# Kernel tuning notes

Measured on AMD Instinct MI355X. Metric: run time of the kernel, lower is better.

## Reference

```python
import jax, jax.numpy as jnp
import numpy as np

I, H, P, B = 1024, 2048, 512, 8192


def setup_inputs() -> dict:
    key = jax.random.key(0)
    ks = jax.random.split(key, 8)
    return {
        "input": jax.random.normal(ks[0], (B, I), dtype=jnp.float32),
        "hx": jax.random.normal(ks[1], (B, P), dtype=jnp.float32),
        "cx": jax.random.normal(ks[2], (B, H), dtype=jnp.float32),
        # gate params stacked in (i, f, c, o) order -> [4H, ...]
        "w_x": jax.random.normal(ks[3], (4 * H, I), dtype=jnp.float32),
        "b_x": jax.random.normal(ks[4], (4 * H,), dtype=jnp.float32),
        "w_h": jax.random.normal(ks[5], (4 * H, P), dtype=jnp.float32),
        "b_h": jax.random.normal(ks[6], (4 * H,), dtype=jnp.float32),
        "w_proj": jax.random.normal(ks[7], (P, H), dtype=jnp.float32),
    }


def reference(input, hx, cx, w_x, b_x, w_h, b_h, w_proj):
    # One fused GEMM per operand instead of 8 small ones; same math.
    # gates: [B, 4H]
    gates = input @ w_x.T + b_x + hx @ w_h.T + b_h
    i_g, f_g, c_g, o_g = jnp.split(gates, 4, axis=-1)  # each [B, H]
    # NOTE: original module applies NO sigmoid/tanh to the gates (faithful).
    ct = f_g * cx + i_g * c_g                 # [B, H]
    ht = (o_g * jnp.tanh(ct)) @ w_proj.T       # [B, P]
    return (ht, ct)
```

## Files before the change

kernel.cpp:

```cpp
#include <hip/hip_runtime.h>
#include <math.h>
#include <stdint.h>

#define DI static __device__ __forceinline__

typedef __bf16 bf16x8 __attribute__((ext_vector_type(8)));
typedef float f32x4 __attribute__((ext_vector_type(4)));
typedef float float4v __attribute__((ext_vector_type(4)));
typedef unsigned short u16;
typedef unsigned short u16x4 __attribute__((ext_vector_type(4)));

DI float b2f(u16 s) {
    unsigned u = ((unsigned)s) << 16;
    float f;
    __builtin_memcpy(&f, &u, 4);
    return f;
}
DI u16 f2b(float f) {
    unsigned x;
    __builtin_memcpy(&x, &f, 4);
    unsigned r = x + 0x7FFFu + ((x >> 16) & 1u);
    return (u16)(r >> 16);
}

DI void gl_lds(const u16* g, u16* l) {
    __builtin_amdgcn_global_load_lds(
        (__attribute__((address_space(1))) void*)g,
        (__attribute__((address_space(3))) void*)l,
        16, 0, 0);
}

DI float fast_tanh(float x) {
    float xc = fminf(fmaxf(x, -15.f), 15.f);
    float e = __expf(2.0f * xc);
    return (e - 1.f) / (e + 1.f);
}

__global__ void pack_A(const float* __restrict__ inp, const float* __restrict__ hx,
                       u16* __restrict__ Ahi, u16* __restrict__ Alo) {
    const int r = blockIdx.x;
    const int k = threadIdx.x * 4;
    float4v v = (k < 1024) ? *(const float4v*)(inp + (size_t)r * 1024 + k)
                           : *(const float4v*)(hx + (size_t)r * 512 + (k - 1024));
    u16x4 h, l;
#pragma unroll
    for (int e = 0; e < 4; ++e) {
        h[e] = f2b(v[e]);
        l[e] = f2b(v[e] - b2f(h[e]));
    }
    *(u16x4*)(Ahi + (size_t)r * 1536 + k) = h;
    *(u16x4*)(Alo + (size_t)r * 1536 + k) = l;
}

__global__ void pack_W(const float* __restrict__ wx, const float* __restrict__ wh,
                       u16* __restrict__ Whi, u16* __restrict__ Wlo) {
    const int g = blockIdx.x;
    const int k = threadIdx.x * 4;
    float4v v = (k < 1024) ? *(const float4v*)(wx + (size_t)g * 1024 + k)
                           : *(const float4v*)(wh + (size_t)g * 512 + (k - 1024));
    u16x4 h, l;
#pragma unroll
    for (int e = 0; e < 4; ++e) {
        h[e] = f2b(v[e]);
        l[e] = f2b(v[e] - b2f(h[e]));
    }
    *(u16x4*)(Whi + (size_t)g * 1536 + k) = h;
    int lr = -1;
    if (g < 2048) lr = g;
    else if (g >= 4096 && g < 6144) lr = g - 2048;
    if (lr >= 0) *(u16x4*)(Wlo + (size_t)lr * 1536 + k) = l;
}

__global__ void pack_flat_bf16(const float* __restrict__ src, u16* __restrict__ dst) {
    const size_t t = ((size_t)blockIdx.x * blockDim.x + threadIdx.x) * 4;
    float4v v = *(const float4v*)(src + t);
    u16x4 o;
#pragma unroll
    for (int e = 0; e < 4; ++e) o[e] = f2b(v[e]);
    *(u16x4*)(dst + t) = o;
}

DI void swizzle2048(int id, int& bx, int& by) {
    const int xcd = id & 7;
    const int j = id >> 3;
    bx = xcd * 4 + (j & 3);
    by = j >> 2;
}

__global__ __launch_bounds__(256, 2) void gemm_fo(const u16* __restrict__ A,
                                                  const u16* __restrict__ W,
                                                  const float* __restrict__ bxv,
                                                  const float* __restrict__ bhv,
                                                  u16* __restrict__ out) {
    constexpr int K = 1536, BK = 32;
    constexpr int AB = 128 * BK;
    __shared__ u16 As[2 * AB];
    __shared__ u16 Ws[2 * AB];

    const int tid = threadIdx.x, wave = tid >> 6, lane = tid & 63;
    int bxi, byi;
    swizzle2048(blockIdx.x, bxi, byi);
    const size_t tileM = (size_t)byi * 128;
    const size_t wrow0 = (bxi < 16) ? (2048 + (size_t)bxi * 128)
                                    : (6144 + (size_t)(bxi - 16) * 128);
    const size_t ncol0 = (size_t)bxi * 128;
    const int waveM = (wave >> 1) * 64;
    const int waveN = (wave & 1) * 64;

    const int srow = lane >> 2, scol = (lane & 3) * 8;
    const u16* Ag = A + (tileM + (size_t)(wave * 16 + srow)) * K + scol;
    const u16* Wg = W + (wrow0 + (size_t)(wave * 16 + srow)) * K + scol;
    const int lA0 = (wave * 16) * BK;
    const int lA1 = (wave * 16 + 64) * BK;

    f32x4 acc[4][4] = {};
    const int arow = waveM + (lane & 15);
    const int wrow = waveN + (lane & 15);
    const int kq = (lane >> 4) * 8;

#define STAGE_FO(b, k0)                              \
    do {                                             \
        gl_lds(Ag + (k0), &As[(b)*AB + lA0]);        \
        gl_lds(Ag + (size_t)64 * K + (k0), &As[(b)*AB + lA1]); \
        gl_lds(Wg + (k0), &Ws[(b)*AB + lA0]);        \
        gl_lds(Wg + (size_t)64 * K + (k0), &Ws[(b)*AB + lA1]); \
    } while (0)

#define COMPUTE_FO(b)                                                          \
    do {                                                                       \
        bf16x8 af[4], wf[4];                                                   \
        _Pragma("unroll") for (int i = 0; i < 4; ++i)                          \
            af[i] = *(const bf16x8*)&As[(b)*AB + (arow + i * 16) * BK + kq];   \
        _Pragma("unroll") for (int j = 0; j < 4; ++j)                          \
            wf[j] = *(const bf16x8*)&Ws[(b)*AB + (wrow + j * 16) * BK + kq];   \
        _Pragma("unroll") for (int i = 0; i < 4; ++i)                          \
            _Pragma("unroll") for (int j = 0; j < 4; ++j)                      \
                acc[i][j] = __builtin_amdgcn_mfma_f32_16x16x32_bf16(           \
                    af[i], wf[j], acc[i][j], 0, 0, 0);                         \
    } while (0)

    STAGE_FO(0, 0);
    __syncthreads();
    for (int k0 = 0; k0 < K; k0 += 2 * BK) {
        STAGE_FO(1, k0 + BK);
        COMPUTE_FO(0);
        __syncthreads();
        if (k0 + 2 * BK < K) STAGE_FO(0, k0 + 2 * BK);
        COMPUTE_FO(1);
        __syncthreads();
    }
#undef STAGE_FO
#undef COMPUTE_FO

    const int rq = (lane >> 4) * 4;
#pragma unroll
    for (int i = 0; i < 4; ++i) {
        const size_t rbase = tileM + waveM + i * 16 + rq;
#pragma unroll
        for (int j = 0; j < 4; ++j) {
            const int nl = waveN + (lane & 15) + j * 16;
            const float bias = bxv[wrow0 + nl] + bhv[wrow0 + nl];
#pragma unroll
            for (int v = 0; v < 4; ++v)
                out[(rbase + v) * 4096 + ncol0 + nl] = f2b(acc[i][j][v] + bias);
        }
    }
}

__global__ __launch_bounds__(256, 2) void gemm_ic_cell(
    const u16* __restrict__ Ahi, const u16* __restrict__ Alo,
    const u16* __restrict__ Whi, const u16* __restrict__ Wlo,
    const float* __restrict__ bxv, const float* __restrict__ bhv,
    const u16* __restrict__ Gfo, const float* __restrict__ cx,
    float* __restrict__ ct, u16* __restrict__ U) {
    constexpr int K = 1536, BK = 32;
    constexpr int AB = 128 * BK;
    constexpr int WB = 64 * BK;
    __shared__ u16 sAh[2 * AB], sAl[2 * AB];
    __shared__ u16 sWih[2 * WB], sWil[2 * WB], sWch[2 * WB], sWcl[2 * WB];

    const int tid = threadIdx.x, wave = tid >> 6, lane = tid & 63;
    int bxi, byi;
    swizzle2048(blockIdx.x, bxi, byi);
    const size_t tileM = (size_t)byi * 128;
    const size_t h0 = (size_t)bxi * 64;
    const int waveM = (wave >> 1) * 64;
    const int waveH = (wave & 1) * 32;

    const int srow = lane >> 2, scol = (lane & 3) * 8;
    const size_t wr = (size_t)(wave * 16 + srow);
    const u16* gAh = Ahi + (tileM + wr) * K + scol;
    const u16* gAl = Alo + (tileM + wr) * K + scol;
    const u16* gWih = Whi + (h0 + wr) * K + scol;
    const u16* gWch = Whi + (4096 + h0 + wr) * K + scol;
    const u16* gWil = Wlo + (h0 + wr) * K + scol;
    const u16* gWcl = Wlo + (2048 + h0 + wr) * K + scol;
    const int lA0 = (wave * 16) * BK;
    const int lA1 = (wave * 16 + 64) * BK;
    const int lW0 = (wave * 16) * BK;

    f32x4 ai[4][2] = {}, ac[4][2] = {};
    const int arow = waveM + (lane & 15);
    const int wrow = waveH + (lane & 15);
    const int kq = (lane >> 4) * 8;

#define STAGE_IC(b, k0)                                          \
    do {                                                         \
        gl_lds(gAh + (k0), &sAh[(b)*AB + lA0]);                  \
        gl_lds(gAh + (size_t)64 * K + (k0), &sAh[(b)*AB + lA1]); \
        gl_lds(gAl + (k0), &sAl[(b)*AB + lA0]);                  \
        gl_lds(gAl + (size_t)64 * K + (k0), &sAl[(b)*AB + lA1]); \
        gl_lds(gWih + (k0), &sWih[(b)*WB + lW0]);                \
        gl_lds(gWil + (k0), &sWil[(b)*WB + lW0]);                \
        gl_lds(gWch + (k0), &sWch[(b)*WB + lW0]);                \
        gl_lds(gWcl + (k0), &sWcl[(b)*WB + lW0]);                \
    } while (0)

#define COMPUTE_IC(b)                                                            \
    do {                                                                         \
        bf16x8 ah[4], al[4], wih[2], wil[2], wch[2], wcl[2];                     \
        _Pragma("unroll") for (int i = 0; i < 4; ++i) {                          \
            ah[i] = *(const bf16x8*)&sAh[(b)*AB + (arow + i * 16) * BK + kq];    \
            al[i] = *(const bf16x8*)&sAl[(b)*AB + (arow + i * 16) * BK + kq];    \
        }                                                                        \
        _Pragma("unroll") for (int j = 0; j < 2; ++j) {                          \
            wih[j] = *(const bf16x8*)&sWih[(b)*WB + (wrow + j * 16) * BK + kq];  \
            wil[j] = *(const bf16x8*)&sWil[(b)*WB + (wrow + j * 16) * BK + kq];  \
            wch[j] = *(const bf16x8*)&sWch[(b)*WB + (wrow + j * 16) * BK + kq];  \
            wcl[j] = *(const bf16x8*)&sWcl[(b)*WB + (wrow + j * 16) * BK + kq];  \
        }                                                                        \
        _Pragma("unroll") for (int i = 0; i < 4; ++i)                            \
            _Pragma("unroll") for (int j = 0; j < 2; ++j) {                      \
                ai[i][j] = __builtin_amdgcn_mfma_f32_16x16x32_bf16(ah[i], wih[j], ai[i][j], 0, 0, 0); \
                ai[i][j] = __builtin_amdgcn_mfma_f32_16x16x32_bf16(al[i], wih[j], ai[i][j], 0, 0, 0); \
                ai[i][j] = __builtin_amdgcn_mfma_f32_16x16x32_bf16(ah[i], wil[j], ai[i][j], 0, 0, 0); \
                ac[i][j] = __builtin_amdgcn_mfma_f32_16x16x32_bf16(ah[i], wch[j], ac[i][j], 0, 0, 0); \
                ac[i][j] = __builtin_amdgcn_mfma_f32_16x16x32_bf16(al[i], wch[j], ac[i][j], 0, 0, 0); \
                ac[i][j] = __builtin_amdgcn_mfma_f32_16x16x32_bf16(ah[i], wcl[j], ac[i][j], 0, 0, 0); \
            }                                                                    \
    } while (0)

    STAGE_IC(0, 0);
    __syncthreads();
    for (int k0 = 0; k0 < K; k0 += 2 * BK) {
        STAGE_IC(1, k0 + BK);
        COMPUTE_IC(0);
        __syncthreads();
        if (k0 + 2 * BK < K) STAGE_IC(0, k0 + 2 * BK);
        COMPUTE_IC(1);
        __syncthreads();
    }
#undef STAGE_IC
#undef COMPUTE_IC

    const int rq = (lane >> 4) * 4;
#pragma unroll
    for (int j = 0; j < 2; ++j) {
        const size_t h = h0 + waveH + j * 16 + (lane & 15);
        const float bi = bxv[h] + bhv[h];
        const float bc = bxv[4096 + h] + bhv[4096 + h];
#pragma unroll
        for (int i = 0; i < 4; ++i) {
            const size_t m0 = tileM + waveM + i * 16 + rq;
#pragma unroll
            for (int v = 0; v < 4; ++v) {
                const size_t m = m0 + v;
                const float iv = ai[i][j][v] + bi;
                const float cv = ac[i][j][v] + bc;
                const float f = b2f(Gfo[m * 4096 + h]);
                const float o = b2f(Gfo[m * 4096 + 2048 + h]);
                const float c_ = f * cx[m * 2048 + h] + iv * cv;
                ct[m * 2048 + h] = c_;
                U[m * 2048 + h] = f2b(o * fast_tanh(c_));
            }
        }
    }
}

__global__ __launch_bounds__(256, 2) void gemm_proj(const u16* __restrict__ A,
                                                    const u16* __restrict__ W,
                                                    float* __restrict__ out) {
    constexpr int K = 2048, BK = 32;
    constexpr int AB = 128 * BK;
    constexpr int WB = 64 * BK;
    __shared__ u16 As[2 * AB];
    __shared__ u16 Ws[2 * WB];

    const int tid = threadIdx.x, wave = tid >> 6, lane = tid & 63;
    const size_t tileM = (size_t)blockIdx.y * 128;
    const size_t tileN = (size_t)blockIdx.x * 64;
    const int waveM = (wave >> 1) * 64;
    const int waveN = (wave & 1) * 32;

    const int srow = lane >> 2, scol = (lane & 3) * 8;
    const u16* Ag = A + (tileM + (size_t)(wave * 16 + srow)) * K + scol;
    const u16* Wg = W + (tileN + (size_t)(wave * 16 + srow)) * K + scol;
    const int lA0 = (wave * 16) * BK;
    const int lA1 = (wave * 16 + 64) * BK;

    f32x4 acc[4][2] = {};
    const int arow = waveM + (lane & 15);
    const int wrow = waveN + (lane & 15);
    const int kq = (lane >> 4) * 8;

#define STAGE_PR(b, k0)                                        \
    do {                                                       \
        gl_lds(Ag + (k0), &As[(b)*AB + lA0]);                  \
        gl_lds(Ag + (size_t)64 * K + (k0), &As[(b)*AB + lA1]); \
        gl_lds(Wg + (k0), &Ws[(b)*WB + lA0]);                  \
    } while (0)

#define COMPUTE_PR(b)                                                          \
    do {                                                                       \
        bf16x8 af[4], wf[2];                                                   \
        _Pragma("unroll") for (int i = 0; i < 4; ++i)                          \
            af[i] = *(const bf16x8*)&As[(b)*AB + (arow + i * 16) * BK + kq];   \
        _Pragma("unroll") for (int j = 0; j < 2; ++j)                          \
            wf[j] = *(const bf16x8*)&Ws[(b)*WB + (wrow + j * 16) * BK + kq];   \
        _Pragma("unroll") for (int i = 0; i < 4; ++i)                          \
            _Pragma("unroll") for (int j = 0; j < 2; ++j)                      \
                acc[i][j] = __builtin_amdgcn_mfma_f32_16x16x32_bf16(           \
                    af[i], wf[j], acc[i][j], 0, 0, 0);                         \
    } while (0)

    STAGE_PR(0, 0);
    __syncthreads();
    for (int k0 = 0; k0 < K; k0 += 2 * BK) {
        STAGE_PR(1, k0 + BK);
        COMPUTE_PR(0);
        __syncthreads();
        if (k0 + 2 * BK < K) STAGE_PR(0, k0 + 2 * BK);
        COMPUTE_PR(1);
        __syncthreads();
    }
#undef STAGE_PR
#undef COMPUTE_PR

    const int rq = (lane >> 4) * 4;
#pragma unroll
    for (int i = 0; i < 4; ++i) {
        const size_t rbase = tileM + waveM + i * 16 + rq;
#pragma unroll
        for (int j = 0; j < 2; ++j) {
            const size_t n = tileN + waveN + (lane & 15) + j * 16;
#pragma unroll
            for (int v = 0; v < 4; ++v)
                out[(rbase + v) * 512 + n] = acc[i][j][v];
        }
    }
}

extern "C" void kernel_launch(void* const* d_in, const int* in_sizes, int n_in,
                              void* d_out, int out_size, void* d_ws, size_t ws_size,
                              hipStream_t stream) {
    const float* input  = (const float*)d_in[0];
    const float* hx     = (const float*)d_in[1];
    const float* cx     = (const float*)d_in[2];
    const float* w_x    = (const float*)d_in[3];
    const float* b_x    = (const float*)d_in[4];
    const float* w_h    = (const float*)d_in[5];
    const float* b_h    = (const float*)d_in[6];
    const float* w_proj = (const float*)d_in[7];

    constexpr int H = 2048, P = 512, B = 8192;

    char* ws = (char*)d_ws;
    u16* Ahi = (u16*)(ws);
    u16* Alo = (u16*)(ws + 25165824);
    u16* Whi = (u16*)(ws + 50331648);
    u16* Wlo = (u16*)(ws + 75497472);
    u16* Gfo = (u16*)(ws + 88080384);
    u16* U   = (u16*)(ws + 155189248);
    u16* Wp  = (u16*)(ws + 188743680);

    float* ht = (float*)d_out;
    float* ct = (float*)d_out + (size_t)B * P;

    pack_A<<<B, 384, 0, stream>>>(input, hx, Ahi, Alo);
    pack_W<<<4 * H, 384, 0, stream>>>(w_x, w_h, Whi, Wlo);
    pack_flat_bf16<<<(P * H / 4) / 256, 256, 0, stream>>>(w_proj, Wp);

    gemm_fo<<<2048, 256, 0, stream>>>(Ahi, Whi, b_x, b_h, Gfo);
    gemm_ic_cell<<<2048, 256, 0, stream>>>(Ahi, Alo, Whi, Wlo, b_x, b_h,
                                           Gfo, cx, ct, U);
    gemm_proj<<<dim3(8, 64), 256, 0, stream>>>(U, Wp, ht);
}
```

Baseline: 711.7 us.

## Rewrite gate GEMMs as 256x256 8-wave tiles with swizzled LDS and phased pipeline

Replaces the two gate GEMM kernels with 512-thread blocks that compute 256x256 output tiles, using a BK=64 XOR-swizzled LDS layout and a hand-scheduled loop. That loop interleaves global-to-LDS staging with quarter-tile MFMA phases, using explicit vmcnt waits, s_setprio and sched barriers. The i/c kernel now treats the hi/lo split-precision products as one long K loop over concatenated segments. The i and c results go to different waves and are combined through LDS in the epilogue. The aim is more data reuse per byte loaded and better overlap of memory with MFMA, at the cost of much more complex scheduling, a 128KB LDS footprint and high register pressure.

Result: slower. 860.5 us (+20.9%).

```diff
diff --git a/kernel.cpp b/kernel.cpp
--- a/kernel.cpp
+++ b/kernel.cpp
@@ -1,6 +1,7 @@
 #include <hip/hip_runtime.h>
 #include <math.h>
 #include <stdint.h>
+
 
 #define DI static __device__ __forceinline__
 
@@ -80,198 +81,278 @@
     *(u16x4*)(dst + t) = o;
 }
 
-DI void swizzle2048(int id, int& bx, int& by) {
-    const int xcd = id & 7;
-    const int j = id >> 3;
-    bx = xcd * 4 + (j & 3);
-    by = j >> 2;
-}
-
-__global__ __launch_bounds__(256, 2) void gemm_fo(const u16* __restrict__ A,
-                                                  const u16* __restrict__ W,
-                                                  const float* __restrict__ bxv,
-                                                  const float* __restrict__ bhv,
-                                                  u16* __restrict__ out) {
-    constexpr int K = 1536, BK = 32;
-    constexpr int AB = 128 * BK;
-    __shared__ u16 As[2 * AB];
-    __shared__ u16 Ws[2 * AB];
-
-    const int tid = threadIdx.x, wave = tid >> 6, lane = tid & 63;
-    int bxi, byi;
-    swizzle2048(blockIdx.x, bxi, byi);
-    const size_t tileM = (size_t)byi * 128;
-    const size_t wrow0 = (bxi < 16) ? (2048 + (size_t)bxi * 128)
-                                    : (6144 + (size_t)(bxi - 16) * 128);
-    const size_t ncol0 = (size_t)bxi * 128;
-    const int waveM = (wave >> 1) * 64;
-    const int waveN = (wave & 1) * 64;
-
-    const int srow = lane >> 2, scol = (lane & 3) * 8;
-    const u16* Ag = A + (tileM + (size_t)(wave * 16 + srow)) * K + scol;
-    const u16* Wg = W + (wrow0 + (size_t)(wave * 16 + srow)) * K + scol;
-    const int lA0 = (wave * 16) * BK;
-    const int lA1 = (wave * 16 + 64) * BK;
-
-    f32x4 acc[4][4] = {};
-    const int arow = waveM + (lane & 15);
-    const int wrow = waveN + (lane & 15);
-    const int kq = (lane >> 4) * 8;
-
-#define STAGE_FO(b, k0)                              \
-    do {                                             \
-        gl_lds(Ag + (k0), &As[(b)*AB + lA0]);        \
-        gl_lds(Ag + (size_t)64 * K + (k0), &As[(b)*AB + lA1]); \
-        gl_lds(Wg + (k0), &Ws[(b)*AB + lA0]);        \
-        gl_lds(Wg + (size_t)64 * K + (k0), &Ws[(b)*AB + lA1]); \
-    } while (0)
-
-#define COMPUTE_FO(b)                                                          \
-    do {                                                                       \
-        bf16x8 af[4], wf[4];                                                   \
-        _Pragma("unroll") for (int i = 0; i < 4; ++i)                          \
-            af[i] = *(const bf16x8*)&As[(b)*AB + (arow + i * 16) * BK + kq];   \
-        _Pragma("unroll") for (int j = 0; j < 4; ++j)                          \
-            wf[j] = *(const bf16x8*)&Ws[(b)*AB + (wrow + j * 16) * BK + kq];   \
-        _Pragma("unroll") for (int i = 0; i < 4; ++i)                          \
-            _Pragma("unroll") for (int j = 0; j < 4; ++j)                      \
-                acc[i][j] = __builtin_amdgcn_mfma_f32_16x16x32_bf16(           \
-                    af[i], wf[j], acc[i][j], 0, 0, 0);                         \
-    } while (0)
-
-    STAGE_FO(0, 0);
-    __syncthreads();
-    for (int k0 = 0; k0 < K; k0 += 2 * BK) {
-        STAGE_FO(1, k0 + BK);
-        COMPUTE_FO(0);
-        __syncthreads();
-        if (k0 + 2 * BK < K) STAGE_FO(0, k0 + 2 * BK);
-        COMPUTE_FO(1);
-        __syncthreads();
-    }
-#undef STAGE_FO
-#undef COMPUTE_FO
-
-    const int rq = (lane >> 4) * 4;
-#pragma unroll
-    for (int i = 0; i < 4; ++i) {
-        const size_t rbase = tileM + waveM + i * 16 + rq;
-#pragma unroll
-        for (int j = 0; j < 4; ++j) {
-            const int nl = waveN + (lane & 15) + j * 16;
-            const float bias = bxv[wrow0 + nl] + bhv[wrow0 + nl];
+
+#define PH_FENCE() __builtin_amdgcn_sched_barrier(0)
+#define PH_BAR()                           \
+    do {                                   \
+        PH_FENCE();                        \
+        __builtin_amdgcn_s_barrier();      \
+        PH_FENCE();                        \
+    } while (0)
+#define VMCNT(n) asm volatile("s_waitcnt vmcnt(" #n ")" ::: "memory")
+
+#define LDA_(b, mh)                                                                   \
+    do {                                                                              \
+        _Pragma("unroll") for (int i_ = 0; i_ < 4; ++i_) {                            \
+            Af[i_][0] = *(const bf16x8*)(pA + (b)*16384 + ((mh)*4 + i_) * 1024 + cs0);\
+            Af[i_][1] = *(const bf16x8*)(pA + (b)*16384 + ((mh)*4 + i_) * 1024 + cs1);\
+        }                                                                             \
+    } while (0)
+
+#define LDW_(b, jj)                                                                   \
+    do {                                                                              \
+        _Pragma("unroll") for (int j_ = 0; j_ < 2; ++j_) {                            \
+            Wf[(jj)*2 + j_][0] =                                                      \
+                *(const bf16x8*)(pW + (b)*16384 + ((jj)*2 + j_) * 1024 + cs0);        \
+            Wf[(jj)*2 + j_][1] =                                                      \
+                *(const bf16x8*)(pW + (b)*16384 + ((jj)*2 + j_) * 1024 + cs1);        \
+        }                                                                             \
+    } while (0)
+
+#define MFMAQ(mh, nh)                                                                 \
+    do {                                                                              \
+        __builtin_amdgcn_s_setprio(1);                                                \
+        _Pragma("unroll") for (int i_ = 0; i_ < 4; ++i_) {                            \
+            _Pragma("unroll") for (int j_ = 0; j_ < 2; ++j_) {                        \
+                acc[(mh)*4 + i_][(nh)*2 + j_] =                                       \
+                    __builtin_amdgcn_mfma_f32_16x16x32_bf16(                          \
+                        Af[i_][0], Wf[(nh)*2 + j_][0],                                \
+                        acc[(mh)*4 + i_][(nh)*2 + j_], 0, 0, 0);                      \
+                acc[(mh)*4 + i_][(nh)*2 + j_] =                                       \
+                    __builtin_amdgcn_mfma_f32_16x16x32_bf16(                          \
+                        Af[i_][1], Wf[(nh)*2 + j_][1],                                \
+                        acc[(mh)*4 + i_][(nh)*2 + j_], 0, 0, 0);                      \
+            }                                                                         \
+        }                                                                             \
+        __builtin_amdgcn_s_setprio(0);                                                \
+    } while (0)
+
+#define GEMM8_LOOP(NI_, SA, SW)                                                       \
+    SA(0, 0, 0);                                                                      \
+    SA(0, 0, 1);                                                                      \
+    SW(0, 0, 0);                                                                      \
+    SW(0, 0, 1);                                                                      \
+    SW(1, 1, 0);                                                                      \
+    SA(1, 1, 0);                                                                      \
+    VMCNT(4);                                                                         \
+    PH_BAR();                                                                         \
+    for (int I_ = 0; I_ < (NI_); ++I_) {                                              \
+        const int t_ = 2 * I_;                                                        \
+        const bool more_ = (I_ < (NI_)-1);                                            \
+                                                                              \
+        LDA_(0, 0);                                                                   \
+        LDW_(0, 0);                                                                   \
+        SW(1, t_ + 1, 1);                                                             \
+        PH_BAR();                                                                     \
+        MFMAQ(0, 0);                                                                  \
+        PH_BAR();                                                                     \
+                                                                              \
+        LDW_(0, 1);                                                                   \
+        SA(1, t_ + 1, 1);                                                             \
+        PH_BAR();                                                                     \
+        MFMAQ(0, 1);                                                                  \
+        PH_BAR();                                                                     \
+                                                                              \
+        LDA_(0, 1);                                                                   \
+        if (more_) SW(0, t_ + 2, 0);                                                  \
+        PH_BAR();                                                                     \
+        MFMAQ(1, 0);                                                                  \
+        PH_BAR();                                                                     \
+                                                                              \
+        if (more_) SW(0, t_ + 2, 1);                                                  \
+        PH_BAR();                                                                     \
+        MFMAQ(1, 1);                                                                  \
+        PH_FENCE();                                                                   \
+        if (more_) { VMCNT(4); } else { VMCNT(0); }                                   \
+        PH_BAR();                                                                     \
+                                                                              \
+        LDA_(1, 0);                                                                   \
+        LDW_(1, 0);                                                                   \
+        if (more_) SA(0, t_ + 2, 0);                                                  \
+        PH_BAR();                                                                     \
+        MFMAQ(0, 0);                                                                  \
+        PH_BAR();                                                                     \
+                                                                              \
+        LDW_(1, 1);                                                                   \
+        if (more_) SA(0, t_ + 2, 1);                                                  \
+        PH_BAR();                                                                     \
+        MFMAQ(0, 1);                                                                  \
+        PH_BAR();                                                                     \
+                                                                              \
+        LDA_(1, 1);                                                                   \
+        if (more_) SW(1, t_ + 3, 0);                                                  \
+        PH_BAR();                                                                     \
+        MFMAQ(1, 0);                                                                  \
+        PH_BAR();                                                                     \
+                                                                              \
+        if (more_) SA(1, t_ + 3, 0);                                                  \
+        PH_BAR();                                                                     \
+        MFMAQ(1, 1);                                                                  \
+        PH_FENCE();                                                                   \
+        if (more_) {                                                                  \
+            VMCNT(4);                                                                 \
+            PH_BAR();                                                                 \
+        }                                                                             \
+    }
+
+__global__ __launch_bounds__(512, 2) void gemm8_fo(const u16* __restrict__ A,
+                                                   const u16* __restrict__ W,
+                                                   const float* __restrict__ bxv,
+                                                   const float* __restrict__ bhv,
+                                                   u16* __restrict__ out) {
+    constexpr int NKT = 24, NI = NKT / 2;
+    __shared__ u16 sm[65536];
+
+    const int tid = threadIdx.x, wid = tid >> 6, lane = tid & 63;
+    const int wm = wid >> 2, wn = wid & 3;
+    const int id = blockIdx.x;
+    const int wgid = (id & 7) * 64 + (id >> 3);
+    const int mt = wgid >> 4, nt = wgid & 15;
+    const size_t rowA0 = (size_t)mt * 256;
+    const size_t rowW0 = (nt < 8) ? (2048 + (size_t)nt * 256) : (4096 + (size_t)nt * 256);
+
+    const int rl = lane >> 3;
+    const int cl8 = ((lane & 7) ^ rl) * 8;
+    const int r15 = lane & 15, q4 = lane >> 4, x7 = lane & 7;
+    const int cs0 = (q4 ^ x7) * 8;
+    const int cs1 = ((q4 + 4) ^ x7) * 8;
+    u16* pA = sm + ((size_t)wm * 128 + r15) * 64;
+    u16* pW = sm + 32768 + ((size_t)wn * 64 + r15) * 64;
+
+#define STG_A_FO(b, kt, hh)                                                           \
+    do {                                                                              \
+        const u16* s_ = A + (rowA0 + (hh)*128 + wid * 8 + rl) * (size_t)1536 +        \
+                        (kt)*64 + cl8;                                                \
+        u16* d_ = sm + (b)*16384 + ((hh)*128 + wid * 8) * 64;                         \
+        gl_lds(s_, d_);                                                               \
+        gl_lds(s_ + (size_t)64 * 1536, d_ + 4096);                                    \
+    } while (0)
+#define STG_W_FO(b, kt, hh)                                                           \
+    do {                                                                              \
+        const u16* s_ = W + (rowW0 + (hh)*128 + wid * 8 + rl) * (size_t)1536 +        \
+                        (kt)*64 + cl8;                                                \
+        u16* d_ = sm + 32768 + (b)*16384 + ((hh)*128 + wid * 8) * 64;                 \
+        gl_lds(s_, d_);                                                               \
+        gl_lds(s_ + (size_t)64 * 1536, d_ + 4096);                                    \
+    } while (0)
+
+    f32x4 acc[8][4] = {};
+    bf16x8 Af[4][2], Wf[4][2];
+
+    GEMM8_LOOP(NI, STG_A_FO, STG_W_FO);
+#undef STG_A_FO
+#undef STG_W_FO
+
+    const size_t mBase = (size_t)mt * 256 + wm * 128;
+#pragma unroll
+    for (int j = 0; j < 4; ++j) {
+        const size_t n = (size_t)nt * 256 + wn * 64 + j * 16 + r15;
+        const size_t g = (n < 2048) ? (2048 + n) : (4096 + n);
+        const float bias = bxv[g] + bhv[g];
+#pragma unroll
+        for (int i = 0; i < 8; ++i) {
+            const size_t m0 = mBase + i * 16 + q4 * 4;
 #pragma unroll
             for (int v = 0; v < 4; ++v)
-                out[(rbase + v) * 4096 + ncol0 + nl] = f2b(acc[i][j][v] + bias);
+                out[(m0 + v) * 4096 + n] = f2b(acc[i][j][v] + bias);
         }
     }
 }
 
-__global__ __launch_bounds__(256, 2) void gemm_ic_cell(
+__global__ __launch_bounds__(512, 2) void gemm8_ic_cell(
     const u16* __restrict__ Ahi, const u16* __restrict__ Alo,
     const u16* __restrict__ Whi, const u16* __restrict__ Wlo,
     const float* __restrict__ bxv, const float* __restrict__ bhv,
     const u16* __restrict__ Gfo, const float* __restrict__ cx,
     float* __restrict__ ct, u16* __restrict__ U) {
-    constexpr int K = 1536, BK = 32;
-    constexpr int AB = 128 * BK;
-    constexpr int WB = 64 * BK;
-    __shared__ u16 sAh[2 * AB], sAl[2 * AB];
-    __shared__ u16 sWih[2 * WB], sWil[2 * WB], sWch[2 * WB], sWcl[2 * WB];
-
-    const int tid = threadIdx.x, wave = tid >> 6, lane = tid & 63;
-    int bxi, byi;
-    swizzle2048(blockIdx.x, bxi, byi);
-    const size_t tileM = (size_t)byi * 128;
-    const size_t h0 = (size_t)bxi * 64;
-    const int waveM = (wave >> 1) * 64;
-    const int waveH = (wave & 1) * 32;
-
-    const int srow = lane >> 2, scol = (lane & 3) * 8;
-    const size_t wr = (size_t)(wave * 16 + srow);
-    const u16* gAh = Ahi + (tileM + wr) * K + scol;
-    const u16* gAl = Alo + (tileM + wr) * K + scol;
-    const u16* gWih = Whi + (h0 + wr) * K + scol;
-    const u16* gWch = Whi + (4096 + h0 + wr) * K + scol;
-    const u16* gWil = Wlo + (h0 + wr) * K + scol;
-    const u16* gWcl = Wlo + (2048 + h0 + wr) * K + scol;
-    const int lA0 = (wave * 16) * BK;
-    const int lA1 = (wave * 16 + 64) * BK;
-    const int lW0 = (wave * 16) * BK;
-
-    f32x4 ai[4][2] = {}, ac[4][2] = {};
-    const int arow = waveM + (lane & 15);
-    const int wrow = waveH + (lane & 15);
-    const int kq = (lane >> 4) * 8;
-
-#define STAGE_IC(b, k0)                                          \
-    do {                                                         \
-        gl_lds(gAh + (k0), &sAh[(b)*AB + lA0]);                  \
-        gl_lds(gAh + (size_t)64 * K + (k0), &sAh[(b)*AB + lA1]); \
-        gl_lds(gAl + (k0), &sAl[(b)*AB + lA0]);                  \
-        gl_lds(gAl + (size_t)64 * K + (k0), &sAl[(b)*AB + lA1]); \
-        gl_lds(gWih + (k0), &sWih[(b)*WB + lW0]);                \
-        gl_lds(gWil + (k0), &sWil[(b)*WB + lW0]);                \
-        gl_lds(gWch + (k0), &sWch[(b)*WB + lW0]);                \
-        gl_lds(gWcl + (k0), &sWcl[(b)*WB + lW0]);                \
-    } while (0)
-
-#define COMPUTE_IC(b)                                                            \
-    do {                                                                         \
-        bf16x8 ah[4], al[4], wih[2], wil[2], wch[2], wcl[2];                     \
-        _Pragma("unroll") for (int i = 0; i < 4; ++i) {                          \
-            ah[i] = *(const bf16x8*)&sAh[(b)*AB + (arow + i * 16) * BK + kq];    \
-            al[i] = *(const bf16x8*)&sAl[(b)*AB + (arow + i * 16) * BK + kq];    \
-        }                                                                        \
-        _Pragma("unroll") for (int j = 0; j < 2; ++j) {                          \
-            wih[j] = *(const bf16x8*)&sWih[(b)*WB + (wrow + j * 16) * BK + kq];  \
-            wil[j] = *(const bf16x8*)&sWil[(b)*WB + (wrow + j * 16) * BK + kq];  \
-            wch[j] = *(const bf16x8*)&sWch[(b)*WB + (wrow + j * 16) * BK + kq];  \
-            wcl[j] = *(const bf16x8*)&sWcl[(b)*WB + (wrow + j * 16) * BK + kq];  \
-        }                                                                        \
-        _Pragma("unroll") for (int i = 0; i < 4; ++i)                            \
-            _Pragma("unroll") for (int j = 0; j < 2; ++j) {                      \
-                ai[i][j] = __builtin_amdgcn_mfma_f32_16x16x32_bf16(ah[i], wih[j], ai[i][j], 0, 0, 0); \
-                ai[i][j] = __builtin_amdgcn_mfma_f32_16x16x32_bf16(al[i], wih[j], ai[i][j], 0, 0, 0); \
-                ai[i][j] = __builtin_amdgcn_mfma_f32_16x16x32_bf16(ah[i], wil[j], ai[i][j], 0, 0, 0); \
-                ac[i][j] = __builtin_amdgcn_mfma_f32_16x16x32_bf16(ah[i], wch[j], ac[i][j], 0, 0, 0); \
-                ac[i][j] = __builtin_amdgcn_mfma_f32_16x16x32_bf16(al[i], wch[j], ac[i][j], 0, 0, 0); \
-                ac[i][j] = __builtin_amdgcn_mfma_f32_16x16x32_bf16(ah[i], wcl[j], ac[i][j], 0, 0, 0); \
-            }                                                                    \
-    } while (0)
-
-    STAGE_IC(0, 0);
+    constexpr int NKT = 72, NI = NKT / 2;
+    __shared__ u16 sm[65536];
+
+    const int tid = threadIdx.x, wid = tid >> 6, lane = tid & 63;
+    const int wm = wid >> 2, wn = wid & 3;
+    const int id = blockIdx.x;
+    const int wgid = (id & 7) * 64 + (id >> 3);
+    const int mt = wgid >> 4, nt = wgid & 15;
+    const size_t rowA0 = (size_t)mt * 256;
+    const size_t h0t = (size_t)nt * 128;
+
+    const int rl = lane >> 3;
+    const int cl8 = ((lane & 7) ^ rl) * 8;
+    const int r15 = lane & 15, q4 = lane >> 4, x7 = lane & 7;
+    const int cs0 = (q4 ^ x7) * 8;
+    const int cs1 = ((q4 + 4) ^ x7) * 8;
+    u16* pA = sm + ((size_t)wm * 128 + r15) * 64;
+    u16* pW = sm + 32768 + ((size_t)wn * 64 + r15) * 64;
+
+#define STG_A_IC(b, kt, hh)                                                           \
+    do {                                                                              \
+        const int p_ = (kt) / 24;                                                     \
+        const int kc_ = ((kt) % 24) * 64;                                             \
+        const u16* base_ = (p_ == 1) ? Alo : Ahi;                                     \
+        const u16* s_ = base_ + (rowA0 + (hh)*128 + wid * 8 + rl) * (size_t)1536 +    \
+                        kc_ + cl8;                                                    \
+        u16* d_ = sm + (b)*16384 + ((hh)*128 + wid * 8) * 64;                         \
+        gl_lds(s_, d_);                                                               \
+        gl_lds(s_ + (size_t)64 * 1536, d_ + 4096);                                    \
+    } while (0)
+#define STG_W_IC(b, kt, hh)                                                           \
+    do {                                                                              \
+        const int kc_ = ((kt) % 24) * 64;                                             \
+        const u16* wp_ = ((kt) < 48) ? Whi : Wlo;                                     \
+        const size_t rb_ = h0t + ((hh) ? (((kt) < 48) ? (size_t)4096 : (size_t)2048)  \
+                                       : (size_t)0);                                  \
+        const u16* s_ = wp_ + (rb_ + wid * 8 + rl) * (size_t)1536 + kc_ + cl8;        \
+        u16* d_ = sm + 32768 + (b)*16384 + ((hh)*128 + wid * 8) * 64;                 \
+        gl_lds(s_, d_);                                                               \
+        gl_lds(s_ + (size_t)64 * 1536, d_ + 4096);                                    \
+    } while (0)
+
+    f32x4 acc[8][4] = {};
+    bf16x8 Af[4][2], Wf[4][2];
+
+    GEMM8_LOOP(NI, STG_A_IC, STG_W_IC);
+#undef STG_A_IC
+#undef STG_W_IC
+
     __syncthreads();
-    for (int k0 = 0; k0 < K; k0 += 2 * BK) {
-        STAGE_IC(1, k0 + BK);
-        COMPUTE_IC(0);
-        __syncthreads();
-        if (k0 + 2 * BK < K) STAGE_IC(0, k0 + 2 * BK);
-        COMPUTE_IC(1);
-        __syncthreads();
-    }
-#undef STAGE_IC
-#undef COMPUTE_IC
-
-    const int rq = (lane >> 4) * 4;
-#pragma unroll
-    for (int j = 0; j < 2; ++j) {
-        const size_t h = h0 + waveH + j * 16 + (lane & 15);
-        const float bi = bxv[h] + bhv[h];
-        const float bc = bxv[4096 + h] + bhv[4096 + h];
-#pragma unroll
-        for (int i = 0; i < 4; ++i) {
-            const size_t m0 = tileM + waveM + i * 16 + rq;
-#pragma unroll
-            for (int v = 0; v < 4; ++v) {
-                const size_t m = m0 + v;
-                const float iv = ai[i][j][v] + bi;
-                const float cv = ac[i][j][v] + bc;
-                const float f = b2f(Gfo[m * 4096 + h]);
-                const float o = b2f(Gfo[m * 4096 + 2048 + h]);
-                const float c_ = f * cx[m * 2048 + h] + iv * cv;
-                ct[m * 2048 + h] = c_;
-                U[m * 2048 + h] = f2b(o * fast_tanh(c_));
+    float* cb = (float*)sm;
+    const size_t mBase = (size_t)mt * 256 + wm * 128;
+    if (wn >= 2) {
+#pragma unroll
+        for (int j = 0; j < 4; ++j) {
+            const int hl = (wn - 2) * 64 + j * 16 + r15;
+            const size_t h = h0t + hl;
+            const float bc = bxv[4096 + h] + bhv[4096 + h];
+#pragma unroll
+            for (int i = 0; i < 8; ++i) {
+                f32x4 v = acc[i][j];
+                v[0] += bc; v[1] += bc; v[2] += bc; v[3] += bc;
+                *(f32x4*)&cb[(size_t)hl * 256 + wm * 128 + i * 16 + q4 * 4] = v;
+            }
+        }
+    }
+    __syncthreads();
+    if (wn < 2) {
+#pragma unroll
+        for (int j = 0; j < 4; ++j) {
+            const int hl = wn * 64 + j * 16 + r15;
+            const size_t h = h0t + hl;
+            const float bi = bxv[h] + bhv[h];
+#pragma unroll
+            for (int i = 0; i < 8; ++i) {
+                const size_t m0 = mBase + i * 16 + q4 * 4;
+                const f32x4 cv =
+                    *(const f32x4*)&cb[(size_t)hl * 256 + wm * 128 + i * 16 + q4 * 4];
+#pragma unroll
+                for (int v = 0; v < 4; ++v) {
+                    const size_t m = m0 + v;
+                    const float iv = acc[i][j][v] + bi;
+                    const float f = b2f(Gfo[m * 4096 + h]);
+                    const float o = b2f(Gfo[m * 4096 + 2048 + h]);
+                    const float c_ = f * cx[m * 2048 + h] + iv * cv[v];
+                    ct[m * 2048 + h] = c_;
+                    U[m * 2048 + h] = f2b(o * fast_tanh(c_));
+                }
             }
         }
     }
@@ -380,8 +461,8 @@
     pack_W<<<4 * H, 384, 0, stream>>>(w_x, w_h, Whi, Wlo);
     pack_flat_bf16<<<(P * H / 4) / 256, 256, 0, stream>>>(w_proj, Wp);
 
-    gemm_fo<<<2048, 256, 0, stream>>>(Ahi, Whi, b_x, b_h, Gfo);
-    gemm_ic_cell<<<2048, 256, 0, stream>>>(Ahi, Alo, Whi, Wlo, b_x, b_h,
+    gemm8_fo<<<512, 512, 0, stream>>>(Ahi, Whi, b_x, b_h, Gfo);
+    gemm8_ic_cell<<<512, 512, 0, stream>>>(Ahi, Alo, Whi, Wlo, b_x, b_h,
                                            Gfo, cx, ct, U);
     gemm_proj<<<dim3(8, 64), 256, 0, stream>>>(U, Wp, ht);
 }
```

## Fuse forget/output gate GEMM into input/cell gate kernel with cell epilogue

Applied to the files above, without the earlier changes.

Removes the separate gemm_fo kernel and computes the f and o gates inside the cell kernel, alongside i and c, from the same A tiles already staged in LDS. This drops the bf16 Gfo intermediate, a 64MB write followed by a read, and avoids loading the A operand twice. In exchange each block holds four sets of accumulators (64 f32x4 registers) and more LDS for the extra weight tiles. That can cut occupancy below the 2 blocks per CU requested by the launch bounds, or cause register spills.

Result: faster. 642.6 us (-9.7%).

```diff
diff --git a/kernel.cpp b/kernel.cpp
--- a/kernel.cpp
+++ b/kernel.cpp
@@ -1,6 +1,7 @@
 #include <hip/hip_runtime.h>
 #include <math.h>
 #include <stdint.h>
+
 
 #define DI static __device__ __forceinline__
 
@@ -87,96 +88,16 @@
     by = j >> 2;
 }
 
-__global__ __launch_bounds__(256, 2) void gemm_fo(const u16* __restrict__ A,
-                                                  const u16* __restrict__ W,
-                                                  const float* __restrict__ bxv,
-                                                  const float* __restrict__ bhv,
-                                                  u16* __restrict__ out) {
-    constexpr int K = 1536, BK = 32;
-    constexpr int AB = 128 * BK;
-    __shared__ u16 As[2 * AB];
-    __shared__ u16 Ws[2 * AB];
-
-    const int tid = threadIdx.x, wave = tid >> 6, lane = tid & 63;
-    int bxi, byi;
-    swizzle2048(blockIdx.x, bxi, byi);
-    const size_t tileM = (size_t)byi * 128;
-    const size_t wrow0 = (bxi < 16) ? (2048 + (size_t)bxi * 128)
-                                    : (6144 + (size_t)(bxi - 16) * 128);
-    const size_t ncol0 = (size_t)bxi * 128;
-    const int waveM = (wave >> 1) * 64;
-    const int waveN = (wave & 1) * 64;
-
-    const int srow = lane >> 2, scol = (lane & 3) * 8;
-    const u16* Ag = A + (tileM + (size_t)(wave * 16 + srow)) * K + scol;
-    const u16* Wg = W + (wrow0 + (size_t)(wave * 16 + srow)) * K + scol;
-    const int lA0 = (wave * 16) * BK;
-    const int lA1 = (wave * 16 + 64) * BK;
-
-    f32x4 acc[4][4] = {};
-    const int arow = waveM + (lane & 15);
-    const int wrow = waveN + (lane & 15);
-    const int kq = (lane >> 4) * 8;
-
-#define STAGE_FO(b, k0)                              \
-    do {                                             \
-        gl_lds(Ag + (k0), &As[(b)*AB + lA0]);        \
-        gl_lds(Ag + (size_t)64 * K + (k0), &As[(b)*AB + lA1]); \
-        gl_lds(Wg + (k0), &Ws[(b)*AB + lA0]);        \
-        gl_lds(Wg + (size_t)64 * K + (k0), &Ws[(b)*AB + lA1]); \
-    } while (0)
-
-#define COMPUTE_FO(b)                                                          \
-    do {                                                                       \
-        bf16x8 af[4], wf[4];                                                   \
-        _Pragma("unroll") for (int i = 0; i < 4; ++i)                          \
-            af[i] = *(const bf16x8*)&As[(b)*AB + (arow + i * 16) * BK + kq];   \
-        _Pragma("unroll") for (int j = 0; j < 4; ++j)                          \
-            wf[j] = *(const bf16x8*)&Ws[(b)*AB + (wrow + j * 16) * BK + kq];   \
-        _Pragma("unroll") for (int i = 0; i < 4; ++i)                          \
-            _Pragma("unroll") for (int j = 0; j < 4; ++j)                      \
-                acc[i][j] = __builtin_amdgcn_mfma_f32_16x16x32_bf16(           \
-                    af[i], wf[j], acc[i][j], 0, 0, 0);                         \
-    } while (0)
-
-    STAGE_FO(0, 0);
-    __syncthreads();
-    for (int k0 = 0; k0 < K; k0 += 2 * BK) {
-        STAGE_FO(1, k0 + BK);
-        COMPUTE_FO(0);
-        __syncthreads();
-        if (k0 + 2 * BK < K) STAGE_FO(0, k0 + 2 * BK);
-        COMPUTE_FO(1);
-        __syncthreads();
-    }
-#undef STAGE_FO
-#undef COMPUTE_FO
-
-    const int rq = (lane >> 4) * 4;
-#pragma unroll
-    for (int i = 0; i < 4; ++i) {
-        const size_t rbase = tileM + waveM + i * 16 + rq;
-#pragma unroll
-        for (int j = 0; j < 4; ++j) {
-            const int nl = waveN + (lane & 15) + j * 16;
-            const float bias = bxv[wrow0 + nl] + bhv[wrow0 + nl];
-#pragma unroll
-            for (int v = 0; v < 4; ++v)
-                out[(rbase + v) * 4096 + ncol0 + nl] = f2b(acc[i][j][v] + bias);
-        }
-    }
-}
-
-__global__ __launch_bounds__(256, 2) void gemm_ic_cell(
+__global__ __launch_bounds__(256, 2) void gemm_gates_cell(
     const u16* __restrict__ Ahi, const u16* __restrict__ Alo,
     const u16* __restrict__ Whi, const u16* __restrict__ Wlo,
     const float* __restrict__ bxv, const float* __restrict__ bhv,
-    const u16* __restrict__ Gfo, const float* __restrict__ cx,
-    float* __restrict__ ct, u16* __restrict__ U) {
+    const float* __restrict__ cx, float* __restrict__ ct, u16* __restrict__ U) {
     constexpr int K = 1536, BK = 32;
     constexpr int AB = 128 * BK;
     constexpr int WB = 64 * BK;
     __shared__ u16 sAh[2 * AB], sAl[2 * AB];
+    __shared__ u16 sWf[2 * WB], sWo[2 * WB];
     __shared__ u16 sWih[2 * WB], sWil[2 * WB], sWch[2 * WB], sWcl[2 * WB];
 
     const int tid = threadIdx.x, wave = tid >> 6, lane = tid & 63;
@@ -192,86 +113,127 @@
     const u16* gAh = Ahi + (tileM + wr) * K + scol;
     const u16* gAl = Alo + (tileM + wr) * K + scol;
     const u16* gWih = Whi + (h0 + wr) * K + scol;
+    const u16* gWf  = Whi + (2048 + h0 + wr) * K + scol;
     const u16* gWch = Whi + (4096 + h0 + wr) * K + scol;
+    const u16* gWo  = Whi + (6144 + h0 + wr) * K + scol;
     const u16* gWil = Wlo + (h0 + wr) * K + scol;
     const u16* gWcl = Wlo + (2048 + h0 + wr) * K + scol;
     const int lA0 = (wave * 16) * BK;
     const int lA1 = (wave * 16 + 64) * BK;
     const int lW0 = (wave * 16) * BK;
 
-    f32x4 ai[4][2] = {}, ac[4][2] = {};
+    f32x4 aF[4][2] = {}, aO[4][2] = {}, aI[4][2] = {}, aC[4][2] = {};
     const int arow = waveM + (lane & 15);
     const int wrow = waveH + (lane & 15);
     const int kq = (lane >> 4) * 8;
 
-#define STAGE_IC(b, k0)                                          \
+#define STAGE_G(b, k0)                                           \
     do {                                                         \
         gl_lds(gAh + (k0), &sAh[(b)*AB + lA0]);                  \
         gl_lds(gAh + (size_t)64 * K + (k0), &sAh[(b)*AB + lA1]); \
         gl_lds(gAl + (k0), &sAl[(b)*AB + lA0]);                  \
         gl_lds(gAl + (size_t)64 * K + (k0), &sAl[(b)*AB + lA1]); \
+        gl_lds(gWf + (k0), &sWf[(b)*WB + lW0]);                  \
+        gl_lds(gWo + (k0), &sWo[(b)*WB + lW0]);                  \
         gl_lds(gWih + (k0), &sWih[(b)*WB + lW0]);                \
         gl_lds(gWil + (k0), &sWil[(b)*WB + lW0]);                \
         gl_lds(gWch + (k0), &sWch[(b)*WB + lW0]);                \
         gl_lds(gWcl + (k0), &sWcl[(b)*WB + lW0]);                \
     } while (0)
 
-#define COMPUTE_IC(b)                                                            \
-    do {                                                                         \
-        bf16x8 ah[4], al[4], wih[2], wil[2], wch[2], wcl[2];                     \
-        _Pragma("unroll") for (int i = 0; i < 4; ++i) {                          \
-            ah[i] = *(const bf16x8*)&sAh[(b)*AB + (arow + i * 16) * BK + kq];    \
-            al[i] = *(const bf16x8*)&sAl[(b)*AB + (arow + i * 16) * BK + kq];    \
-        }                                                                        \
-        _Pragma("unroll") for (int j = 0; j < 2; ++j) {                          \
-            wih[j] = *(const bf16x8*)&sWih[(b)*WB + (wrow + j * 16) * BK + kq];  \
-            wil[j] = *(const bf16x8*)&sWil[(b)*WB + (wrow + j * 16) * BK + kq];  \
-            wch[j] = *(const bf16x8*)&sWch[(b)*WB + (wrow + j * 16) * BK + kq];  \
-            wcl[j] = *(const bf16x8*)&sWcl[(b)*WB + (wrow + j * 16) * BK + kq];  \
-        }                                                                        \
-        _Pragma("unroll") for (int i = 0; i < 4; ++i)                            \
-            _Pragma("unroll") for (int j = 0; j < 2; ++j) {                      \
-                ai[i][j] = __builtin_amdgcn_mfma_f32_16x16x32_bf16(ah[i], wih[j], ai[i][j], 0, 0, 0); \
-                ai[i][j] = __builtin_amdgcn_mfma_f32_16x16x32_bf16(al[i], wih[j], ai[i][j], 0, 0, 0); \
-                ai[i][j] = __builtin_amdgcn_mfma_f32_16x16x32_bf16(ah[i], wil[j], ai[i][j], 0, 0, 0); \
-                ac[i][j] = __builtin_amdgcn_mfma_f32_16x16x32_bf16(ah[i], wch[j], ac[i][j], 0, 0, 0); \
-                ac[i][j] = __builtin_amdgcn_mfma_f32_16x16x32_bf16(al[i], wch[j], ac[i][j], 0, 0, 0); \
-                ac[i][j] = __builtin_amdgcn_mfma_f32_16x16x32_bf16(ah[i], wcl[j], ac[i][j], 0, 0, 0); \
-            }                                                                    \
+#define COMPUTE_G(b)                                                              \
+    do {                                                                          \
+        bf16x8 ah[4], al[4];                                                      \
+        _Pragma("unroll") for (int i = 0; i < 4; ++i) {                           \
+            ah[i] = *(const bf16x8*)&sAh[(b)*AB + (arow + i * 16) * BK + kq];     \
+            al[i] = *(const bf16x8*)&sAl[(b)*AB + (arow + i * 16) * BK + kq];     \
+        }                                                                         \
+        {                                                     \
+            bf16x8 w[2];                                                          \
+            _Pragma("unroll") for (int j = 0; j < 2; ++j)                         \
+                w[j] = *(const bf16x8*)&sWf[(b)*WB + (wrow + j * 16) * BK + kq];  \
+            _Pragma("unroll") for (int i = 0; i < 4; ++i)                         \
+                _Pragma("unroll") for (int j = 0; j < 2; ++j)                     \
+                    aF[i][j] = __builtin_amdgcn_mfma_f32_16x16x32_bf16(           \
+                        ah[i], w[j], aF[i][j], 0, 0, 0);                          \
+        }                                                                         \
+        {                                                     \
+            bf16x8 w[2];                                                          \
+            _Pragma("unroll") for (int j = 0; j < 2; ++j)                         \
+                w[j] = *(const bf16x8*)&sWo[(b)*WB + (wrow + j * 16) * BK + kq];  \
+            _Pragma("unroll") for (int i = 0; i < 4; ++i)                         \
+                _Pragma("unroll") for (int j = 0; j < 2; ++j)                     \
+                    aO[i][j] = __builtin_amdgcn_mfma_f32_16x16x32_bf16(           \
+                        ah[i], w[j], aO[i][j], 0, 0, 0);                          \
+        }                                                                         \
+        {                                                    \
+            bf16x8 wh[2], wl[2];                                                  \
+            _Pragma("unroll") for (int j = 0; j < 2; ++j) {                       \
+                wh[j] = *(const bf16x8*)&sWih[(b)*WB + (wrow + j * 16) * BK + kq];\
+                wl[j] = *(const bf16x8*)&sWil[(b)*WB + (wrow + j * 16) * BK + kq];\
+            }                                                                     \
+            _Pragma("unroll") for (int i = 0; i < 4; ++i)                         \
+                _Pragma("unroll") for (int j = 0; j < 2; ++j) {                   \
+                    aI[i][j] = __builtin_amdgcn_mfma_f32_16x16x32_bf16(           \
+                        ah[i], wh[j], aI[i][j], 0, 0, 0);                         \
+                    aI[i][j] = __builtin_amdgcn_mfma_f32_16x16x32_bf16(           \
+                        al[i], wh[j], aI[i][j], 0, 0, 0);                         \
+                    aI[i][j] = __builtin_amdgcn_mfma_f32_16x16x32_bf16(           \
+                        ah[i], wl[j], aI[i][j], 0, 0, 0);                         \
+                }                                                                 \
+        }                                                                         \
+        {                                                    \
+            bf16x8 wh[2], wl[2];                                                  \
+            _Pragma("unroll") for (int j = 0; j < 2; ++j) {                       \
+                wh[j] = *(const bf16x8*)&sWch[(b)*WB + (wrow + j * 16) * BK + kq];\
+                wl[j] = *(const bf16x8*)&sWcl[(b)*WB + (wrow + j * 16) * BK + kq];\
+            }                                                                     \
+            _Pragma("unroll") for (int i = 0; i < 4; ++i)                         \
+                _Pragma("unroll") for (int j = 0; j < 2; ++j) {                   \
+                    aC[i][j] = __builtin_amdgcn_mfma_f32_16x16x32_bf16(           \
+                        ah[i], wh[j], aC[i][j], 0, 0, 0);                         \
+                    aC[i][j] = __builtin_amdgcn_mfma_f32_16x16x32_bf16(           \
+                        al[i], wh[j], aC[i][j], 0, 0, 0);                         \
+                    aC[i][j] = __builtin_amdgcn_mfma_f32_16x16x32_bf16(           \
+                        ah[i], wl[j], aC[i][j], 0, 0, 0);                         \
+                }                                                                 \
+        }                                                                         \
     } while (0)
 
-    STAGE_IC(0, 0);
+    STAGE_G(0, 0);
     __syncthreads();
     for (int k0 = 0; k0 < K; k0 += 2 * BK) {
-        STAGE_IC(1, k0 + BK);
-        COMPUTE_IC(0);
+        STAGE_G(1, k0 + BK);
+        COMPUTE_G(0);
         __syncthreads();
-        if (k0 + 2 * BK < K) STAGE_IC(0, k0 + 2 * BK);
-        COMPUTE_IC(1);
+        if (k0 + 2 * BK < K) STAGE_G(0, k0 + 2 * BK);
+        COMPUTE_G(1);
         __syncthreads();
     }
-#undef STAGE_IC
-#undef COMPUTE_IC
+#undef STAGE_G
+#undef COMPUTE_G
 
     const int rq = (lane >> 4) * 4;
 #pragma unroll
     for (int j = 0; j < 2; ++j) {
         const size_t h = h0 + waveH + j * 16 + (lane & 15);
         const float bi = bxv[h] + bhv[h];
+        const float bf = bxv[2048 + h] + bhv[2048 + h];
         const float bc = bxv[4096 + h] + bhv[4096 + h];
+        const float bo = bxv[6144 + h] + bhv[6144 + h];
 #pragma unroll
         for (int i = 0; i < 4; ++i) {
             const size_t m0 = tileM + waveM + i * 16 + rq;
 #pragma unroll
             for (int v = 0; v < 4; ++v) {
                 const size_t m = m0 + v;
-                const float iv = ai[i][j][v] + bi;
-                const float cv = ac[i][j][v] + bc;
-                const float f = b2f(Gfo[m * 4096 + h]);
-                const float o = b2f(Gfo[m * 4096 + 2048 + h]);
-                const float c_ = f * cx[m * 2048 + h] + iv * cv;
+                const float fv = aF[i][j][v] + bf;
+                const float ov = aO[i][j][v] + bo;
+                const float iv = aI[i][j][v] + bi;
+                const float cv = aC[i][j][v] + bc;
+                const float c_ = fv * cx[m * 2048 + h] + iv * cv;
                 ct[m * 2048 + h] = c_;
-                U[m * 2048 + h] = f2b(o * fast_tanh(c_));
+                U[m * 2048 + h] = f2b(ov * fast_tanh(c_));
             }
         }
     }
@@ -369,7 +331,6 @@
     u16* Alo = (u16*)(ws + 25165824);
     u16* Whi = (u16*)(ws + 50331648);
     u16* Wlo = (u16*)(ws + 75497472);
-    u16* Gfo = (u16*)(ws + 88080384);
     u16* U   = (u16*)(ws + 155189248);
     u16* Wp  = (u16*)(ws + 188743680);
 
@@ -380,8 +341,7 @@
     pack_W<<<4 * H, 384, 0, stream>>>(w_x, w_h, Whi, Wlo);
     pack_flat_bf16<<<(P * H / 4) / 256, 256, 0, stream>>>(w_proj, Wp);
 
-    gemm_fo<<<2048, 256, 0, stream>>>(Ahi, Whi, b_x, b_h, Gfo);
-    gemm_ic_cell<<<2048, 256, 0, stream>>>(Ahi, Alo, Whi, Wlo, b_x, b_h,
-                                           Gfo, cx, ct, U);
+    gemm_gates_cell<<<2048, 256, 0, stream>>>(Ahi, Alo, Whi, Wlo, b_x, b_h,
+                                              cx, ct, U);
     gemm_proj<<<dim3(8, 64), 256, 0, stream>>>(U, Wp, ht);
 }
```
